# Kernel optimization log

Hardware: AMD Instinct MI355X
Metric: run time of the kernel (lower is better)

The kernel has to match this reference:

```python
import jax, jax.numpy as jnp
import numpy as np

N = 100000
C_IN = 128
C_OUT = 128
N_EDGE_TYPE = 7
N_SAMPLES = 2
E = 700000


def setup_inputs() -> dict:
    key = jax.random.key(0)
    k1, k2, k3, k4 = jax.random.split(key, 4)
    x = jax.random.normal(k1, (N, C_IN), dtype=jnp.float32)
    col = jax.random.randint(k2, (E,), 0, N, dtype=jnp.int64)
    # per-edge slot index = row * n_edge_type + edge_type, sorted (select_k_sorted needs sorted idx)
    index_sorted = jnp.sort(jax.random.randint(k3, (E,), 0, N * N_EDGE_TYPE, dtype=jnp.int64))
    weights = jax.random.normal(k4, (N_EDGE_TYPE * C_IN, C_OUT), dtype=jnp.float32)
    return {"x": x, "col": col, "index_sorted": index_sorted, "weights": weights}


def reference(x, col, index_sorted, weights):
    n, c = x.shape
    S = n * N_EDGE_TYPE  # total (node, edge_type) slots
    # group stats over the sorted slot index (replaces unique_consecutive + counts)
    counts = jax.ops.segment_sum(jnp.ones_like(index_sorted, dtype=jnp.int32),
                                 index_sorted, num_segments=S)
    starts = jnp.cumsum(counts) - counts  # first edge position of each slot
    # Monte Carlo: sample N_SAMPLES edges (with replacement) per slot
    rel = jax.random.randint(jax.random.key(42), (S, N_SAMPLES), 0, 1 << 30, dtype=jnp.int32)
    rel = rel % jnp.maximum(counts, 1)[:, None]
    gidx = starts[:, None] + rel              # [S, k] indices into the edge list
    x_col = x[col]                            # [E, C] neighbor features
    gathered = x_col[gidx]                    # [S, k, C]
    gathered = jnp.where((counts > 0)[:, None, None], gathered, jnp.zeros((), x.dtype))
    col_data = gathered.mean(axis=1)          # [S, C]
    # self slot (edge_type = n_edge_type-1) is overwritten with the node's own feature
    self_idx = jnp.arange(n) * N_EDGE_TYPE + (N_EDGE_TYPE - 1)
    col_data = col_data.at[self_idx].set(x)
    return col_data.reshape(n, N_EDGE_TYPE * c) @ weights
```

## Files before the change

kernel.cpp:

```cpp
#include <hip/hip_runtime.h>
#include <hip/hip_bf16.h>
#include <stdint.h>

#define N_NODES 100000
#define C 128
#define NET 7
#define E_EDGES 700000
#define S_SLOTS (N_NODES * NET)
#define BM 64
#define NB_CVTX 6250
#define NB_CVTW 56
#define NB_INIT ((S_SLOTS + 255) / 256)

typedef __attribute__((ext_vector_type(8))) short short8;
typedef __attribute__((ext_vector_type(4))) float f32x4;
typedef __attribute__((ext_vector_type(4))) unsigned int uint4v;

struct TF2 { uint32_t a, b; };

__host__ __device__ constexpr uint32_t rotl32c(uint32_t v, int r) {
    return (v << r) | (v >> (32 - r));
}

__host__ __device__ constexpr TF2 threefry2x32(uint32_t k0, uint32_t k1,
                                               uint32_t x0, uint32_t x1) {
    const uint32_t ks0 = k0, ks1 = k1, ks2 = 0x1BD11BDAu ^ k0 ^ k1;
    x0 += ks0; x1 += ks1;
#define RND(r) { x0 += x1; x1 = rotl32c(x1, (r)); x1 ^= x0; }
    RND(13) RND(15) RND(26) RND(6)
    x0 += ks1; x1 += ks2 + 1u;
    RND(17) RND(29) RND(16) RND(24)
    x0 += ks2; x1 += ks0 + 2u;
    RND(13) RND(15) RND(26) RND(6)
    x0 += ks0; x1 += ks1 + 3u;
    RND(17) RND(29) RND(16) RND(24)
    x0 += ks1; x1 += ks2 + 4u;
    RND(13) RND(15) RND(26) RND(6)
    x0 += ks2; x1 += ks0 + 5u;
#undef RND
    return TF2{x0, x1};
}

constexpr TF2 K2 = threefry2x32(0u, 42u, 0u, 1u);

__device__ __forceinline__ uint32_t jax_bits32(uint32_t f) {
    TF2 o = threefry2x32(K2.a, K2.b, 0u, f);
    return o.a ^ o.b;
}

__device__ __forceinline__ unsigned short f2bf(float f) {
    uint32_t u = __float_as_uint(f);
    u += 0x7fffu + ((u >> 16) & 1u);
    return (unsigned short)(u >> 16);
}

__device__ __forceinline__ uint32_t sumpack(uint32_t a, uint32_t b) {
    float alo = __uint_as_float(a << 16);
    float ahi = __uint_as_float(a & 0xffff0000u);
    float blo = __uint_as_float(b << 16);
    float bhi = __uint_as_float(b & 0xffff0000u);
    return (__float_as_uint(ahi + bhi) & 0xffff0000u) | (__float_as_uint(alo + blo) >> 16);
}

__device__ __forceinline__ uint4v sumpack4(uint4v a, uint4v b) {
    uint4v o;
    o.x = sumpack(a.x, b.x); o.y = sumpack(a.y, b.y);
    o.z = sumpack(a.z, b.z); o.w = sumpack(a.w, b.w);
    return o;
}

__global__ __launch_bounds__(256) void prep1(const float* __restrict__ x,
                                             const float* __restrict__ W,
                                             unsigned short* __restrict__ xb,
                                             unsigned short* __restrict__ Wf,
                                             int2* __restrict__ pairs) {
    const int b = blockIdx.x;
    if (b < NB_CVTX) {
        int i = b * 256 + threadIdx.x;
        const float4* src = (const float4*)x + (size_t)i * 2;
        float4 a = src[0], v = src[1];
        union { unsigned short u[8]; uint4v q; } o;
        o.u[0] = f2bf(a.x); o.u[1] = f2bf(a.y); o.u[2] = f2bf(a.z); o.u[3] = f2bf(a.w);
        o.u[4] = f2bf(v.x); o.u[5] = f2bf(v.y); o.u[6] = f2bf(v.z); o.u[7] = f2bf(v.w);
        ((uint4v*)xb)[i] = o.q;
    } else if (b < NB_CVTX + NB_CVTW) {
        int t = (b - NB_CVTX) * 256 + threadIdx.x;
        int l = t & 63, ks = (t >> 6) & 3, n16 = (t >> 8) & 7, et = t >> 11;
        int n = n16 * 16 + (l & 15);
        int k0 = ks * 32 + (l >> 4) * 8;
        union { unsigned short u[8]; uint4v q; } o;
#pragma unroll
        for (int j = 0; j < 8; j++)
            o.u[j] = f2bf(0.5f * W[(size_t)(et * 128 + k0 + j) * 128 + n]);
        ((uint4v*)Wf)[t] = o.q;
    } else {
        int s = (b - NB_CVTX - NB_CVTW) * 256 + threadIdx.x;
        if (s >= S_SLOTS) return;
        int node = s / NET;
        pairs[s] = (s - node * NET == NET - 1) ? make_int2(node, node)
                                               : make_int2(-1, -1);
    }
}

__global__ __launch_bounds__(256) void prep2(const int* __restrict__ idx,
                                             const int* __restrict__ col,
                                             int2* __restrict__ pairs) {
    int e = blockIdx.x * 256 + threadIdx.x;
    if (e >= E_EDGES) return;
    int s = idx[e];
    if (e > 0 && idx[e - 1] == s) return;
    int len = 1;
    while (e + len < E_EDGES && idx[e + len] == s) ++len;
    if (s % NET == NET - 1) return;
    uint32_t b0 = jax_bits32((uint32_t)s * 2u + 0u) & 0x3FFFFFFFu;
    uint32_t b1 = jax_bits32((uint32_t)s * 2u + 1u) & 0x3FFFFFFFu;
    pairs[s] = make_int2(col[e + (int)(b0 % (uint32_t)len)],
                         col[e + (int)(b1 % (uint32_t)len)]);
}

__global__ __launch_bounds__(512, 4) void fused_mfma(const unsigned short* __restrict__ xb,
                                                     const int2* __restrict__ pairs,
                                                     const unsigned short* __restrict__ Wf,
                                                     float* __restrict__ out) {
    __shared__ unsigned char Alds[2][BM * 256];
    const int tid  = threadIdx.x;
    const int nb   = blockIdx.x * BM;
    const int wave = tid >> 6, lane = tid & 63;
    const int lr   = lane & 15, lg = lane >> 4;
    const char* xbc = (const char*)xb;

    const int srow = tid >> 3;
    const int q16  = (tid & 7) * 16;
    const int arow = nb + srow;
    const int prow = (arow < N_NODES) ? arow * NET : -1;
    const int sa0  = srow * 256 + ((q16 >> 4) ^ (srow & 7)) * 16;
    const int sa1  = sa0 + 128;

    uint4v g0[3][2], g1[3][2];
    short8 bfr[2][4];

#define GLOAD(SET, PV) { \
    int2 p_ = (PV); \
    if (p_.x >= 0) { \
        const char* b0_ = xbc + ((size_t)p_.x << 8); \
        const char* b1_ = xbc + ((size_t)p_.y << 8); \
        g0[SET][0] = *(const uint4v*)(b0_ + q16); \
        g0[SET][1] = *(const uint4v*)(b0_ + 128 + q16); \
        g1[SET][0] = *(const uint4v*)(b1_ + q16); \
        g1[SET][1] = *(const uint4v*)(b1_ + 128 + q16); \
    } else { \
        uint4v z_ = {0u, 0u, 0u, 0u}; \
        g0[SET][0] = z_; g0[SET][1] = z_; g1[SET][0] = z_; g1[SET][1] = z_; } }

#define COMBINE(SET, BUF) { \
    uint4v v0_ = sumpack4(g0[SET][0], g1[SET][0]); \
    uint4v v1_ = sumpack4(g0[SET][1], g1[SET][1]); \
    *(uint4v*)(&Alds[BUF][sa0]) = v0_; \
    *(uint4v*)(&Alds[BUF][sa1]) = v1_; }

#define LOADB(DST, ET) { _Pragma("unroll") \
    for (int ks_ = 0; ks_ < 4; ks_++) \
        (DST)[ks_] = *(const short8*)(Wf \
            + (size_t)((((ET) * 8 + wave) * 4 + ks_) * 512) + lane * 8); }

#define BARRIER() { \
    asm volatile("s_waitcnt lgkmcnt(0)" ::: "memory"); \
    __builtin_amdgcn_s_barrier(); \
    __builtin_amdgcn_sched_barrier(0); }

    f32x4 acc[4];
#pragma unroll
    for (int i = 0; i < 4; i++) acc[i] = (f32x4)0.f;

    int2 pj[7];
#pragma unroll
    for (int j = 0; j < 7; j++)
        pj[j] = (prow >= 0) ? pairs[prow + j] : make_int2(-1, -1);

    GLOAD(0, pj[0])
    GLOAD(1, pj[1])
    GLOAD(2, pj[2])
    LOADB(bfr[0], 0)
    COMBINE(0, 0)
    GLOAD(0, pj[3])
    BARRIER()

#pragma unroll
    for (int et = 0; et < NET; ++et) {
        const int cur = et & 1;

        if (et + 1 < NET) LOADB(bfr[cur ^ 1], et + 1)

        if (et >= 1 && et + 3 < NET) GLOAD(et % 3, pj[et + 3])

        if (et + 1 < NET) COMBINE((et + 1) % 3, cur ^ 1)

#pragma unroll
        for (int ks = 0; ks < 4; ks++) {
            const int coff = (((ks * 4 + lg) ^ (lr & 7)) << 4);
            short8 b_ = bfr[cur][ks];
#pragma unroll
            for (int fm = 0; fm < 4; fm++) {
                short8 a_ = *(const short8*)(&Alds[cur][(fm * 16 + lr) * 256 + coff]);
                acc[fm] = __builtin_amdgcn_mfma_f32_16x16x32_bf16(a_, b_, acc[fm], 0, 0, 0);
            }
        }

        if (et + 1 < NET) BARRIER()
    }

#pragma unroll
    for (int fm = 0; fm < 4; fm++) {
        int row0 = nb + fm * 16 + lg * 4;
        int colo = wave * 16 + lr;
#pragma unroll
        for (int j = 0; j < 4; j++)
            if (row0 + j < N_NODES)
                out[(size_t)(row0 + j) * C + colo] = acc[fm][j];
    }
#undef GLOAD
#undef COMBINE
#undef LOADB
#undef BARRIER
}

extern "C" void kernel_launch(void* const* d_in, const int* in_sizes, int n_in,
                              void* d_out, int out_size, void* d_ws, size_t ws_size,
                              hipStream_t stream) {
    const float* x   = (const float*)d_in[0];
    const int*   col = (const int*)d_in[1];
    const int*   idx = (const int*)d_in[2];
    const float* W   = (const float*)d_in[3];
    float* out = (float*)d_out;

    int2* pairs        = (int2*)d_ws;
    unsigned short* xb = (unsigned short*)((char*)pairs + (size_t)S_SLOTS * 8);
    unsigned short* Wf = xb + (size_t)N_NODES * C;

    prep1<<<NB_CVTX + NB_CVTW + NB_INIT, 256, 0, stream>>>(x, W, xb, Wf, pairs);
    prep2<<<(E_EDGES + 255) / 256, 256, 0, stream>>>(idx, col, pairs);
    fused_mfma<<<(N_NODES + BM - 1) / BM, 512, 0, stream>>>(xb, pairs, Wf, out);
}
```

Measured before the change: 75.01 us.

## Shrink fused MFMA block to two waves with 64x64 per-wave output tiles

The fused gather+GEMM kernel goes from 8 waves (each computing a 64x16 output strip) to 2 waves that each compute a 64x64 strip with a 4x4 accumulator grid. Each A fragment read from LDS is now reused across four MFMAs instead of one. Gathers become two threads per row, each loading eight 16-byte chunks per neighbour, and the B operand is streamed in quarter-K phases. This cuts LDS traffic and barrier cost per MFMA, but it uses more registers per thread and leaves fewer waves per block to hide the latency of the random gathers.

```diff
diff --git a/kernel.cpp b/kernel.cpp
--- a/kernel.cpp
+++ b/kernel.cpp
@@ -118,109 +118,112 @@
                          col[e + (int)(b1 % (uint32_t)len)]);
 }
 
-__global__ __launch_bounds__(512, 4) void fused_mfma(const unsigned short* __restrict__ xb,
-                                                     const int2* __restrict__ pairs,
-                                                     const unsigned short* __restrict__ Wf,
-                                                     float* __restrict__ out) {
+__global__ __launch_bounds__(128) void fused_mfma(const unsigned short* __restrict__ xb,
+                                                  const int2* __restrict__ pairs,
+                                                  const unsigned short* __restrict__ Wf,
+                                                  float* __restrict__ out) {
     __shared__ unsigned char Alds[2][BM * 256];
     const int tid  = threadIdx.x;
     const int nb   = blockIdx.x * BM;
-    const int wave = tid >> 6, lane = tid & 63;
+    const int w    = tid >> 6, lane = tid & 63;
     const int lr   = lane & 15, lg = lane >> 4;
     const char* xbc = (const char*)xb;
 
-    const int srow = tid >> 3;
-    const int q16  = (tid & 7) * 16;
-    const int arow = nb + srow;
+    const int r    = tid >> 1, h = tid & 1;
+    const int arow = nb + r;
     const int prow = (arow < N_NODES) ? arow * NET : -1;
-    const int sa0  = srow * 256 + ((q16 >> 4) ^ (srow & 7)) * 16;
-    const int sa1  = sa0 + 128;
-
-    uint4v g0[3][2], g1[3][2];
+    const size_t hoff = (size_t)(h * 128);
+    const int h8 = h * 8, rx = r & 7, wb = r * 256;
+
+    uint4v g0[8], g1[8];
     short8 bfr[2][4];
 
-#define GLOAD(SET, PV) { \
+#define GLOAD(PV) { \
     int2 p_ = (PV); \
     if (p_.x >= 0) { \
-        const char* b0_ = xbc + ((size_t)p_.x << 8); \
-        const char* b1_ = xbc + ((size_t)p_.y << 8); \
-        g0[SET][0] = *(const uint4v*)(b0_ + q16); \
-        g0[SET][1] = *(const uint4v*)(b0_ + 128 + q16); \
-        g1[SET][0] = *(const uint4v*)(b1_ + q16); \
-        g1[SET][1] = *(const uint4v*)(b1_ + 128 + q16); \
+        const uint4v* s0_ = (const uint4v*)(xbc + ((size_t)p_.x << 8) + hoff); \
+        const uint4v* s1_ = (const uint4v*)(xbc + ((size_t)p_.y << 8) + hoff); \
+        _Pragma("unroll") \
+        for (int c_ = 0; c_ < 8; c_++) { g0[c_] = s0_[c_]; g1[c_] = s1_[c_]; } \
     } else { \
         uint4v z_ = {0u, 0u, 0u, 0u}; \
-        g0[SET][0] = z_; g0[SET][1] = z_; g1[SET][0] = z_; g1[SET][1] = z_; } }
-
-#define COMBINE(SET, BUF) { \
-    uint4v v0_ = sumpack4(g0[SET][0], g1[SET][0]); \
-    uint4v v1_ = sumpack4(g0[SET][1], g1[SET][1]); \
-    *(uint4v*)(&Alds[BUF][sa0]) = v0_; \
-    *(uint4v*)(&Alds[BUF][sa1]) = v1_; }
-
-#define LOADB(DST, ET) { _Pragma("unroll") \
-    for (int ks_ = 0; ks_ < 4; ks_++) \
-        (DST)[ks_] = *(const short8*)(Wf \
-            + (size_t)((((ET) * 8 + wave) * 4 + ks_) * 512) + lane * 8); }
+        _Pragma("unroll") \
+        for (int c_ = 0; c_ < 8; c_++) { g0[c_] = z_; g1[c_] = z_; } } }
+
+#define COMBINE(BUF) { \
+    _Pragma("unroll") \
+    for (int c_ = 0; c_ < 8; c_++) { \
+        uint4v v_ = sumpack4(g0[c_], g1[c_]); \
+        *(uint4v*)(&Alds[BUF][wb + (((h8 + c_) ^ rx) << 4)]) = v_; } }
+
+#define LOADBQ(DST, PH) { \
+    _Pragma("unroll") \
+    for (int fn_ = 0; fn_ < 4; fn_++) \
+        (DST)[fn_] = *(const short8*)(Wf \
+            + (size_t)((((((PH) >> 2) * 8 + w * 4 + fn_) * 4) + ((PH) & 3)) * 512) \
+            + lane * 8); }
 
 #define BARRIER() { \
     asm volatile("s_waitcnt lgkmcnt(0)" ::: "memory"); \
     __builtin_amdgcn_s_barrier(); \
     __builtin_amdgcn_sched_barrier(0); }
 
-    f32x4 acc[4];
-#pragma unroll
-    for (int i = 0; i < 4; i++) acc[i] = (f32x4)0.f;
+    f32x4 acc[4][4];
+#pragma unroll
+    for (int i = 0; i < 4; i++)
+#pragma unroll
+        for (int j = 0; j < 4; j++) acc[i][j] = (f32x4)0.f;
 
     int2 pj[7];
 #pragma unroll
     for (int j = 0; j < 7; j++)
         pj[j] = (prow >= 0) ? pairs[prow + j] : make_int2(-1, -1);
 
-    GLOAD(0, pj[0])
-    GLOAD(1, pj[1])
-    GLOAD(2, pj[2])
-    LOADB(bfr[0], 0)
-    COMBINE(0, 0)
-    GLOAD(0, pj[3])
+    GLOAD(pj[0])
+    LOADBQ(bfr[0], 0)
+    COMBINE(0)
+    GLOAD(pj[1])
     BARRIER()
 
 #pragma unroll
     for (int et = 0; et < NET; ++et) {
         const int cur = et & 1;
-
-        if (et + 1 < NET) LOADB(bfr[cur ^ 1], et + 1)
-
-        if (et >= 1 && et + 3 < NET) GLOAD(et % 3, pj[et + 3])
-
-        if (et + 1 < NET) COMBINE((et + 1) % 3, cur ^ 1)
-
-#pragma unroll
-        for (int ks = 0; ks < 4; ks++) {
-            const int coff = (((ks * 4 + lg) ^ (lr & 7)) << 4);
-            short8 b_ = bfr[cur][ks];
+#pragma unroll
+        for (int q = 0; q < 4; ++q) {
+            const int ph = et * 4 + q;
+            if (ph + 1 < 4 * NET) LOADBQ(bfr[(q + 1) & 1], ph + 1)
+            if (q == 3) {
+                if (et + 1 < NET) COMBINE(cur ^ 1)
+                if (et + 2 < NET) GLOAD(pj[et + 2])
+            }
+            const int coff = (((q * 4 + lg) ^ (lr & 7)) << 4);
 #pragma unroll
             for (int fm = 0; fm < 4; fm++) {
                 short8 a_ = *(const short8*)(&Alds[cur][(fm * 16 + lr) * 256 + coff]);
-                acc[fm] = __builtin_amdgcn_mfma_f32_16x16x32_bf16(a_, b_, acc[fm], 0, 0, 0);
+#pragma unroll
+                for (int fn = 0; fn < 4; fn++)
+                    acc[fm][fn] = __builtin_amdgcn_mfma_f32_16x16x32_bf16(
+                        a_, bfr[q & 1][fn], acc[fm][fn], 0, 0, 0);
             }
         }
-
         if (et + 1 < NET) BARRIER()
     }
 
 #pragma unroll
     for (int fm = 0; fm < 4; fm++) {
         int row0 = nb + fm * 16 + lg * 4;
-        int colo = wave * 16 + lr;
-#pragma unroll
-        for (int j = 0; j < 4; j++)
-            if (row0 + j < N_NODES)
-                out[(size_t)(row0 + j) * C + colo] = acc[fm][j];
+#pragma unroll
+        for (int fn = 0; fn < 4; fn++) {
+            int colo = w * 64 + fn * 16 + lr;
+#pragma unroll
+            for (int j = 0; j < 4; j++)
+                if (row0 + j < N_NODES)
+                    out[(size_t)(row0 + j) * C + colo] = acc[fm][fn][j];
+        }
     }
 #undef GLOAD
 #undef COMBINE
-#undef LOADB
+#undef LOADBQ
 #undef BARRIER
 }
 
@@ -239,5 +242,5 @@
 
     prep1<<<NB_CVTX + NB_CVTW + NB_INIT, 256, 0, stream>>>(x, W, xb, Wf, pairs);
     prep2<<<(E_EDGES + 255) / 256, 256, 0, stream>>>(idx, col, pairs);
-    fused_mfma<<<(N_NODES + BM - 1) / BM, 512, 0, stream>>>(xb, pairs, Wf, out);
-}
+    fused_mfma<<<(N_NODES + BM - 1) / BM, 128, 0, stream>>>(xb, pairs, Wf, out);
+}
```

Result: slower. 104.7 us (+39.5%).

## Double row tile to 128 with 1024-thread blocks and 2x2 wave tiling

Applied to the files above, without the earlier changes.

Increases the node tile per block from 64 to 128 rows and launches 1024 threads, arranging 16 waves as a 4x4 grid where each wave computes a 32x32 output sub-tile with 2x2 MFMA fragments. This halves the number of blocks and the per-block reloading of the weight fragments relative to output rows, and improves operand reuse inside each wave (each A fragment feeds two MFMAs). In exchange LDS per block doubles to 64 KB and occupancy per CU may drop, and fewer blocks means less latency hiding for the irregular gather loads.

```diff
diff --git a/kernel.cpp b/kernel.cpp
--- a/kernel.cpp
+++ b/kernel.cpp
@@ -7,7 +7,7 @@
 #define NET 7
 #define E_EDGES 700000
 #define S_SLOTS (N_NODES * NET)
-#define BM 64
+#define BM 128
 #define NB_CVTX 6250
 #define NB_CVTW 56
 #define NB_INIT ((S_SLOTS + 255) / 256)
@@ -118,14 +118,15 @@
                          col[e + (int)(b1 % (uint32_t)len)]);
 }
 
-__global__ __launch_bounds__(512, 4) void fused_mfma(const unsigned short* __restrict__ xb,
-                                                     const int2* __restrict__ pairs,
-                                                     const unsigned short* __restrict__ Wf,
-                                                     float* __restrict__ out) {
+__global__ __launch_bounds__(1024, 4) void fused_mfma(const unsigned short* __restrict__ xb,
+                                                      const int2* __restrict__ pairs,
+                                                      const unsigned short* __restrict__ Wf,
+                                                      float* __restrict__ out) {
     __shared__ unsigned char Alds[2][BM * 256];
     const int tid  = threadIdx.x;
     const int nb   = blockIdx.x * BM;
     const int wave = tid >> 6, lane = tid & 63;
+    const int wr   = wave >> 2, wc = wave & 3;
     const int lr   = lane & 15, lg = lane >> 4;
     const char* xbc = (const char*)xb;
 
@@ -137,7 +138,7 @@
     const int sa1  = sa0 + 128;
 
     uint4v g0[3][2], g1[3][2];
-    short8 bfr[2][4];
+    short8 bfr[2][2][4];
 
 #define GLOAD(SET, PV) { \
     int2 p_ = (PV); \
@@ -159,18 +160,21 @@
     *(uint4v*)(&Alds[BUF][sa1]) = v1_; }
 
 #define LOADB(DST, ET) { _Pragma("unroll") \
-    for (int ks_ = 0; ks_ < 4; ks_++) \
-        (DST)[ks_] = *(const short8*)(Wf \
-            + (size_t)((((ET) * 8 + wave) * 4 + ks_) * 512) + lane * 8); }
+    for (int fn_ = 0; fn_ < 2; fn_++) { _Pragma("unroll") \
+        for (int ks_ = 0; ks_ < 4; ks_++) \
+            (DST)[fn_][ks_] = *(const short8*)(Wf \
+                + (size_t)((((ET) * 8 + wc * 2 + fn_) * 4 + ks_) * 512) + lane * 8); } }
 
 #define BARRIER() { \
     asm volatile("s_waitcnt lgkmcnt(0)" ::: "memory"); \
     __builtin_amdgcn_s_barrier(); \
     __builtin_amdgcn_sched_barrier(0); }
 
-    f32x4 acc[4];
-#pragma unroll
-    for (int i = 0; i < 4; i++) acc[i] = (f32x4)0.f;
+    f32x4 acc[2][2];
+#pragma unroll
+    for (int i = 0; i < 2; i++)
+#pragma unroll
+        for (int j = 0; j < 2; j++) acc[i][j] = (f32x4)0.f;
 
     int2 pj[7];
 #pragma unroll
@@ -198,11 +202,13 @@
 #pragma unroll
         for (int ks = 0; ks < 4; ks++) {
             const int coff = (((ks * 4 + lg) ^ (lr & 7)) << 4);
-            short8 b_ = bfr[cur][ks];
-#pragma unroll
-            for (int fm = 0; fm < 4; fm++) {
-                short8 a_ = *(const short8*)(&Alds[cur][(fm * 16 + lr) * 256 + coff]);
-                acc[fm] = __builtin_amdgcn_mfma_f32_16x16x32_bf16(a_, b_, acc[fm], 0, 0, 0);
+#pragma unroll
+            for (int fm = 0; fm < 2; fm++) {
+                short8 a_ = *(const short8*)(&Alds[cur][(wr * 32 + fm * 16 + lr) * 256 + coff]);
+#pragma unroll
+                for (int fn = 0; fn < 2; fn++)
+                    acc[fm][fn] = __builtin_amdgcn_mfma_f32_16x16x32_bf16(
+                        a_, bfr[cur][fn][ks], acc[fm][fn], 0, 0, 0);
             }
         }
 
@@ -210,13 +216,16 @@
     }
 
 #pragma unroll
-    for (int fm = 0; fm < 4; fm++) {
-        int row0 = nb + fm * 16 + lg * 4;
-        int colo = wave * 16 + lr;
-#pragma unroll
-        for (int j = 0; j < 4; j++)
-            if (row0 + j < N_NODES)
-                out[(size_t)(row0 + j) * C + colo] = acc[fm][j];
+    for (int fm = 0; fm < 2; fm++) {
+        int row0 = nb + wr * 32 + fm * 16 + lg * 4;
+#pragma unroll
+        for (int fn = 0; fn < 2; fn++) {
+            int colo = wc * 32 + fn * 16 + lr;
+#pragma unroll
+            for (int j = 0; j < 4; j++)
+                if (row0 + j < N_NODES)
+                    out[(size_t)(row0 + j) * C + colo] = acc[fm][fn][j];
+        }
     }
 #undef GLOAD
 #undef COMBINE
@@ -239,5 +248,5 @@
 
     prep1<<<NB_CVTX + NB_CVTW + NB_INIT, 256, 0, stream>>>(x, W, xb, Wf, pairs);
     prep2<<<(E_EDGES + 255) / 256, 256, 0, stream>>>(idx, col, pairs);
-    fused_mfma<<<(N_NODES + BM - 1) / BM, 512, 0, stream>>>(xb, pairs, Wf, out);
-}
+    fused_mfma<<<(N_NODES + BM - 1) / BM, 1024, 0, stream>>>(xb, pairs, Wf, out);
+}
```

Result: slower. 163.5 us (+118.0%).

## Merge prep kernels, skip duplicate neighbor gathers, and raise MFMA priority

Applied to the files above, without the earlier changes.

The two prep kernels become one launch. A memset zero-fills the pairs buffer, so the per-slot init pass is gone, and the self slot is built inside the GEMM kernel instead of stored. Pairs are now stored offset by one. When both samples pick the same neighbor, the second row gather is skipped and the value is doubled by adding to the bf16 exponent bits. This cuts gather traffic for the many single-edge slots, at the cost of a memset and some branching. The MFMA loop is also wrapped in s_setprio to favour the compute waves.

```diff
diff --git a/kernel.cpp b/kernel.cpp
--- a/kernel.cpp
+++ b/kernel.cpp
@@ -10,7 +10,7 @@
 #define BM 64
 #define NB_CVTX 6250
 #define NB_CVTW 56
-#define NB_INIT ((S_SLOTS + 255) / 256)
+#define NB_SCAN ((E_EDGES + 255) / 256)
 
 typedef __attribute__((ext_vector_type(8))) short short8;
 typedef __attribute__((ext_vector_type(4))) float f32x4;
@@ -69,11 +69,13 @@
     return o;
 }
 
-__global__ __launch_bounds__(256) void prep1(const float* __restrict__ x,
-                                             const float* __restrict__ W,
-                                             unsigned short* __restrict__ xb,
-                                             unsigned short* __restrict__ Wf,
-                                             int2* __restrict__ pairs) {
+__global__ __launch_bounds__(256) void prep(const float* __restrict__ x,
+                                            const float* __restrict__ W,
+                                            const int* __restrict__ idx,
+                                            const int* __restrict__ col,
+                                            unsigned short* __restrict__ xb,
+                                            unsigned short* __restrict__ Wf,
+                                            int2* __restrict__ pairs) {
     const int b = blockIdx.x;
     if (b < NB_CVTX) {
         int i = b * 256 + threadIdx.x;
@@ -94,28 +96,20 @@
             o.u[j] = f2bf(0.5f * W[(size_t)(et * 128 + k0 + j) * 128 + n]);
         ((uint4v*)Wf)[t] = o.q;
     } else {
-        int s = (b - NB_CVTX - NB_CVTW) * 256 + threadIdx.x;
-        if (s >= S_SLOTS) return;
-        int node = s / NET;
-        pairs[s] = (s - node * NET == NET - 1) ? make_int2(node, node)
-                                               : make_int2(-1, -1);
+        int e = (b - NB_CVTX - NB_CVTW) * 256 + threadIdx.x;
+        if (e >= E_EDGES) return;
+        int s = idx[e];
+        if (e > 0 && idx[e - 1] == s) return;
+        if (s % NET == NET - 1) return;
+        int len = 1;
+        while (e + len < E_EDGES && idx[e + len] == s) ++len;
+        uint32_t b0 = jax_bits32((uint32_t)s * 2u + 0u) & 0x3FFFFFFFu;
+        uint32_t b1 = jax_bits32((uint32_t)s * 2u + 1u) & 0x3FFFFFFFu;
+        int c0 = col[e + (int)(b0 % (uint32_t)len)];
+        int c1 = col[e + (int)(b1 % (uint32_t)len)];
+        pairs[s] = (c0 == c1) ? make_int2(c0 + 1, 0)
+                              : make_int2(c0 + 1, c1 + 1);
     }
-}
-
-__global__ __launch_bounds__(256) void prep2(const int* __restrict__ idx,
-                                             const int* __restrict__ col,
-                                             int2* __restrict__ pairs) {
-    int e = blockIdx.x * 256 + threadIdx.x;
-    if (e >= E_EDGES) return;
-    int s = idx[e];
-    if (e > 0 && idx[e - 1] == s) return;
-    int len = 1;
-    while (e + len < E_EDGES && idx[e + len] == s) ++len;
-    if (s % NET == NET - 1) return;
-    uint32_t b0 = jax_bits32((uint32_t)s * 2u + 0u) & 0x3FFFFFFFu;
-    uint32_t b1 = jax_bits32((uint32_t)s * 2u + 1u) & 0x3FFFFFFFu;
-    pairs[s] = make_int2(col[e + (int)(b0 % (uint32_t)len)],
-                         col[e + (int)(b1 % (uint32_t)len)]);
 }
 
 __global__ __launch_bounds__(512, 4) void fused_mfma(const unsigned short* __restrict__ xb,
@@ -137,24 +131,34 @@
     const int sa1  = sa0 + 128;
 
     uint4v g0[3][2], g1[3][2];
+    int2   pset[3];
     short8 bfr[2][4];
 
 #define GLOAD(SET, PV) { \
-    int2 p_ = (PV); \
-    if (p_.x >= 0) { \
-        const char* b0_ = xbc + ((size_t)p_.x << 8); \
-        const char* b1_ = xbc + ((size_t)p_.y << 8); \
+    int2 p_ = (PV); pset[SET] = p_; \
+    if (p_.x > 0) { \
+        const char* b0_ = xbc + ((size_t)(p_.x - 1) << 8); \
         g0[SET][0] = *(const uint4v*)(b0_ + q16); \
         g0[SET][1] = *(const uint4v*)(b0_ + 128 + q16); \
-        g1[SET][0] = *(const uint4v*)(b1_ + q16); \
-        g1[SET][1] = *(const uint4v*)(b1_ + 128 + q16); \
+        if (p_.y > 0) { \
+            const char* b1_ = xbc + ((size_t)(p_.y - 1) << 8); \
+            g1[SET][0] = *(const uint4v*)(b1_ + q16); \
+            g1[SET][1] = *(const uint4v*)(b1_ + 128 + q16); \
+        } \
+    } }
+
+#define COMBINE(SET, BUF) { \
+    int2 p_ = pset[SET]; \
+    uint4v v0_, v1_; \
+    if (p_.x <= 0) { \
+        uint4v z_ = {0u, 0u, 0u, 0u}; v0_ = z_; v1_ = z_; \
+    } else if (p_.y <= 0) { \
+        v0_ = g0[SET][0] + 0x00800080u;    \
+        v1_ = g0[SET][1] + 0x00800080u; \
     } else { \
-        uint4v z_ = {0u, 0u, 0u, 0u}; \
-        g0[SET][0] = z_; g0[SET][1] = z_; g1[SET][0] = z_; g1[SET][1] = z_; } }
-
-#define COMBINE(SET, BUF) { \
-    uint4v v0_ = sumpack4(g0[SET][0], g1[SET][0]); \
-    uint4v v1_ = sumpack4(g0[SET][1], g1[SET][1]); \
+        v0_ = sumpack4(g0[SET][0], g1[SET][0]); \
+        v1_ = sumpack4(g0[SET][1], g1[SET][1]); \
+    } \
     *(uint4v*)(&Alds[BUF][sa0]) = v0_; \
     *(uint4v*)(&Alds[BUF][sa1]) = v1_; }
 
@@ -174,8 +178,9 @@
 
     int2 pj[7];
 #pragma unroll
-    for (int j = 0; j < 7; j++)
-        pj[j] = (prow >= 0) ? pairs[prow + j] : make_int2(-1, -1);
+    for (int j = 0; j < 6; j++)
+        pj[j] = (prow >= 0) ? pairs[prow + j] : make_int2(0, 0);
+    pj[6] = (prow >= 0) ? make_int2(arow + 1, 0) : make_int2(0, 0);
 
     GLOAD(0, pj[0])
     GLOAD(1, pj[1])
@@ -195,6 +200,7 @@
 
         if (et + 1 < NET) COMBINE((et + 1) % 3, cur ^ 1)
 
+        __builtin_amdgcn_s_setprio(1);
 #pragma unroll
         for (int ks = 0; ks < 4; ks++) {
             const int coff = (((ks * 4 + lg) ^ (lr & 7)) << 4);
@@ -205,6 +211,7 @@
                 acc[fm] = __builtin_amdgcn_mfma_f32_16x16x32_bf16(a_, b_, acc[fm], 0, 0, 0);
             }
         }
+        __builtin_amdgcn_s_setprio(0);
 
         if (et + 1 < NET) BARRIER()
     }
@@ -237,7 +244,7 @@
     unsigned short* xb = (unsigned short*)((char*)pairs + (size_t)S_SLOTS * 8);
     unsigned short* Wf = xb + (size_t)N_NODES * C;
 
-    prep1<<<NB_CVTX + NB_CVTW + NB_INIT, 256, 0, stream>>>(x, W, xb, Wf, pairs);
-    prep2<<<(E_EDGES + 255) / 256, 256, 0, stream>>>(idx, col, pairs);
+    hipMemsetAsync(pairs, 0, (size_t)S_SLOTS * sizeof(int2), stream);
+    prep<<<NB_CVTX + NB_CVTW + NB_SCAN, 256, 0, stream>>>(x, W, idx, col, xb, Wf, pairs);
     fused_mfma<<<(N_NODES + BM - 1) / BM, 512, 0, stream>>>(xb, pairs, Wf, out);
 }
```

Result: slower. 77.22 us (+2.9%).
